# Performance work log

Hardware: AMD Instinct MI355X
Metric: run time of the kernel (lower is better)

The kernel has to match this reference:

```python
import jax, jax.numpy as jnp
import numpy as np

EMBED_DIM = 1024
NUM_HEADS = 16
HEAD_DIM = EMBED_DIM // NUM_HEADS
BATCH = 2
SEQ = 2048


def setup_inputs() -> dict:
    key = jax.random.key(0)
    ks = jax.random.split(key, 7)
    bound = 1.0 / np.sqrt(EMBED_DIM)  # nn.Linear default init range
    x = jax.random.normal(ks[0], (BATCH, SEQ, EMBED_DIM), dtype=jnp.float32)
    attn_mask = jnp.ones((BATCH, SEQ), dtype=jnp.int32)
    Wq = jax.random.uniform(ks[1], (EMBED_DIM, EMBED_DIM), jnp.float32, -bound, bound)
    bq = jax.random.uniform(ks[2], (EMBED_DIM,), jnp.float32, -bound, bound)
    Wk = jax.random.uniform(ks[3], (EMBED_DIM, EMBED_DIM), jnp.float32, -bound, bound)
    bk = jax.random.uniform(ks[4], (EMBED_DIM,), jnp.float32, -bound, bound)
    Wv = jax.random.uniform(ks[5], (EMBED_DIM, EMBED_DIM), jnp.float32, -bound, bound)
    bv = jax.random.uniform(ks[6], (EMBED_DIM,), jnp.float32, -bound, bound)
    return {"x": x, "attn_mask": attn_mask, "inv_scale": 8,
            "Wq": Wq, "bq": bq, "Wk": Wk, "bk": bk, "Wv": Wv, "bv": bv}


def reference(x, attn_mask, inv_scale, Wq, bq, Wk, bk, Wv, bv):
    bs, seq_len, _ = x.shape
    # Linear layers (torch: y = x @ W.T + b; here W stored as [in,out])
    def split_heads(y):
        return y.reshape(bs, seq_len, NUM_HEADS, HEAD_DIM).transpose(0, 2, 1, 3)  # [b,h,s,d]
    q = split_heads(x @ Wq + bq)
    k = split_heads(x @ Wk + bk)
    v = split_heads(x @ Wv + bv)
    scores = jnp.einsum('bhqd,bhkd->bhqk', q, k) / jnp.asarray(inv_scale, x.dtype)
    mask = (attn_mask == 0)[:, None, None, :]  # True where masked
    scores = jnp.where(mask, -jnp.inf, scores)
    attn = jax.nn.softmax(scores, axis=-1)
    out = jnp.einsum('bhqk,bhkd->bhqd', attn, v)  # [b,h,s,d]
    return out
```

## Files before the change

kernel.cpp:

```cpp
#include <hip/hip_runtime.h>
#include <stdint.h>

typedef __bf16 bf16x8 __attribute__((ext_vector_type(8)));
typedef float f32x4 __attribute__((ext_vector_type(4)));
typedef uint32_t u32x2 __attribute__((ext_vector_type(2)));
typedef uint32_t u32x4 __attribute__((ext_vector_type(4)));

#define MFMA16(a, b, c) __builtin_amdgcn_mfma_f32_16x16x32_bf16((a), (b), (c), 0, 0, 0)

#if __has_builtin(__builtin_amdgcn_exp2f)
#define EXP2F(x) __builtin_amdgcn_exp2f(x)
#else
#define EXP2F(x) exp2f(x)
#endif

__device__ __forceinline__ void gload16(const void* gsrc, void* ldst) {
  __builtin_amdgcn_global_load_lds((__attribute__((address_space(1))) void*)gsrc,
                                   (__attribute__((address_space(3))) void*)ldst, 16, 0, 0);
}

__device__ __forceinline__ uint32_t pkbf(float a, float b) {
  uint16_t ua = __builtin_bit_cast(uint16_t, (__bf16)a);
  uint16_t ub = __builtin_bit_cast(uint16_t, (__bf16)b);
  return (uint32_t)ua | ((uint32_t)ub << 16);
}

__global__ __launch_bounds__(256) void prep_kernel(
    const float* __restrict__ x, const float* __restrict__ Wq,
    const float* __restrict__ Wk, const float* __restrict__ Wv,
    ushort* __restrict__ xb, ushort* __restrict__ wt) {
  int tid = blockIdx.x * 256 + threadIdx.x;
  if (tid < 524288) {
    const f32x4* xp = (const f32x4*)x;
    f32x4 a = xp[tid * 2], b = xp[tid * 2 + 1];
    u32x4 o;
    o[0] = pkbf(a[0], a[1]);
    o[1] = pkbf(a[2], a[3]);
    o[2] = pkbf(b[0], b[1]);
    o[3] = pkbf(b[2], b[3]);
    *(u32x4*)(xb + (size_t)tid * 8) = o;
  } else {
    int r = tid - 524288;
    int mtx = r >> 17;
    int q = r & 131071;
    int n = q & 1023, kc = q >> 10;
    const float* W = (mtx == 0) ? Wq : (mtx == 1) ? Wk : Wv;
    const float* src = W + (size_t)kc * 8 * 1024 + n;
    float v0 = src[0], v1 = src[1024], v2 = src[2048], v3 = src[3072];
    float v4 = src[4096], v5 = src[5120], v6 = src[6144], v7 = src[7168];
    u32x4 o;
    o[0] = pkbf(v0, v1);
    o[1] = pkbf(v2, v3);
    o[2] = pkbf(v4, v5);
    o[3] = pkbf(v6, v7);
    *(u32x4*)(wt + (size_t)mtx * 1048576 + (size_t)n * 1024 + kc * 8) = o;
  }
}

__global__ __launch_bounds__(256, 2) void gemm_qkv(
    const ushort* __restrict__ xb, const ushort* __restrict__ wt,
    const float* __restrict__ bq, const float* __restrict__ bk,
    const float* __restrict__ bv, const int* __restrict__ invp,
    ushort* __restrict__ Qb, ushort* __restrict__ Kb, ushort* __restrict__ Vt) {
  __shared__ ushort ash[2][128 * 64];
  __shared__ ushort bsh[2][128 * 64];
  const int tid = threadIdx.x;
  const int w = tid >> 6, l = tid & 63;
  const int lq = l & 15, g = l >> 4;

  const int f = blockIdx.x;
  const int nf = (f & 7) * 96 + (f >> 3);
  const int bx = nf / 24, byy = nf % 24;
  const int z = byy >> 3;
  const int m0 = bx * 128, n0 = (byy & 7) * 128;

  const ushort* A = xb;
  const ushort* B = wt + (size_t)z * 1048576;
  const float* bias = (z == 0) ? bq : (z == 1) ? bk : bv;
  const float qs = 1.44269504088896341f / (float)(invp[0]);

  const int lr = l >> 3;
  const int scol = ((l & 7) * 8) ^ (lr * 8);
  const int wr = w >> 1, wc = w & 1;
  const int swz = (lq & 7) << 4;

  f32x4 acc[4][4] = {};

  auto stage = [&](int nb, int t) {
    int k0 = t * 64;
#pragma unroll
    for (int i = 0; i < 4; ++i) {
      int row = w * 32 + i * 8;
      gload16(A + (size_t)(m0 + row + lr) * 1024 + k0 + scol, &ash[nb][row * 64]);
    }
#pragma unroll
    for (int i = 0; i < 4; ++i) {
      int row = w * 32 + i * 8;
      gload16(B + (size_t)(n0 + row + lr) * 1024 + k0 + scol, &bsh[nb][row * 64]);
    }
  };

  stage(0, 0);
  __syncthreads();
  int buf = 0;
  for (int t = 0; t < 16; ++t) {
    if (t < 15) stage(buf ^ 1, t + 1);
    bf16x8 af[4][2], bfr[4][2];
#pragma unroll
    for (int mi = 0; mi < 4; ++mi)
#pragma unroll
      for (int kk = 0; kk < 2; ++kk) {
        int row = wr * 64 + mi * 16 + lq;
        af[mi][kk] = *(const bf16x8*)((const char*)&ash[buf][0] + row * 128 +
                                      ((kk * 64 + g * 16) ^ swz));
      }
#pragma unroll
    for (int ni = 0; ni < 4; ++ni)
#pragma unroll
      for (int kk = 0; kk < 2; ++kk) {
        int row = wc * 64 + ni * 16 + lq;
        bfr[ni][kk] = *(const bf16x8*)((const char*)&bsh[buf][0] + row * 128 +
                                       ((kk * 64 + g * 16) ^ swz));
      }
#pragma unroll
    for (int mi = 0; mi < 4; ++mi)
#pragma unroll
      for (int ni = 0; ni < 4; ++ni) {
        acc[mi][ni] = MFMA16(af[mi][0], bfr[ni][0], acc[mi][ni]);
        acc[mi][ni] = MFMA16(af[mi][1], bfr[ni][1], acc[mi][ni]);
      }
    __syncthreads();
    buf ^= 1;
  }

#pragma unroll
  for (int ni = 0; ni < 4; ++ni) {
    int nn = n0 + wc * 64 + ni * 16 + lq;
    int h = nn >> 6, d = nn & 63;
    float bb = bias[nn];
#pragma unroll
    for (int mi = 0; mi < 4; ++mi) {
      int mbase = m0 + wr * 64 + mi * 16 + g * 4;
      if (z < 2) {
        ushort* dst = (z == 0) ? Qb : Kb;
#pragma unroll
        for (int j = 0; j < 4; ++j) {
          int mm = mbase + j;
          int b = mm >> 11, s = mm & 2047;
          float v = acc[mi][ni][j] + bb;
          if (z == 0) v *= qs;
          dst[((size_t)(b * 16 + h) * 2048 + s) * 64 + d] =
              __builtin_bit_cast(uint16_t, (__bf16)v);
        }
      } else {
        int b = mbase >> 11, s0 = mbase & 2047;
        u32x2 pk;
        pk[0] = pkbf(acc[mi][ni][0] + bb, acc[mi][ni][1] + bb);
        pk[1] = pkbf(acc[mi][ni][2] + bb, acc[mi][ni][3] + bb);
        *(u32x2*)(Vt + ((size_t)(b * 16 + h) * 64 + d) * 2048 + s0) = pk;
      }
    }
  }
}

__global__ __launch_bounds__(256, 4) void attn_kernel(
    const ushort* __restrict__ Qb, const ushort* __restrict__ Kb,
    const ushort* __restrict__ Vt, const int* __restrict__ mask,
    float* __restrict__ out) {
  __shared__ ushort ksh[2][64 * 64];
  __shared__ ushort vsh[2][64 * 64];
  __shared__ ushort psh[4][16 * 64];
  const int tid = threadIdx.x;
  const int w = tid >> 6, l = tid & 63;
  const int lq = l & 15, g = l >> 4;

  const int f = blockIdx.x;
  const int nf = ((f & 7) << 7) + (f >> 3);
  const int qt = nf & 31, bh = nf >> 5;
  const int b = bh >> 4;

  const ushort* Qp = Qb + ((size_t)bh * 2048 + qt * 64 + w * 16) * 64;
  const ushort* Kp = Kb + (size_t)bh * 2048 * 64;
  const ushort* Vp = Vt + (size_t)bh * 64 * 2048;
  const int* mp = mask + b * 2048;

  const int lr = l >> 3;
  const int scol = ((l & 7) * 8) ^ (lr * 8);
  const int swz = (lq & 7) << 4;

  bf16x8 qf_[2];
#pragma unroll
  for (int kk = 0; kk < 2; ++kk)
    qf_[kk] = *(const bf16x8*)(Qp + lq * 64 + kk * 32 + g * 8);

  f32x4 acco[4] = {};
  float m_ = -__builtin_inff();
  float l_ = 0.f;

  auto stage = [&](int nb, int t) {
#pragma unroll
    for (int i = 0; i < 2; ++i) {
      int row = w * 16 + i * 8;
      gload16(Kp + (size_t)(t * 64 + row + lr) * 64 + scol, &ksh[nb][row * 64]);
      gload16(Vp + (size_t)(row + lr) * 2048 + t * 64 + scol, &vsh[nb][row * 64]);
    }
  };
  stage(0, 0);
  __syncthreads();
  int buf = 0;
  for (int t = 0; t < 32; ++t) {
    if (t < 31) stage(buf ^ 1, t + 1);
    bf16x8 kf_[4][2];
#pragma unroll
    for (int kf = 0; kf < 4; ++kf)
#pragma unroll
      for (int kk = 0; kk < 2; ++kk) {
        int row = kf * 16 + lq;
        kf_[kf][kk] = *(const bf16x8*)((const char*)&ksh[buf][0] + row * 128 +
                                       ((kk * 64 + g * 16) ^ swz));
      }
    f32x4 sc[4];
    __builtin_amdgcn_s_setprio(1);
#pragma unroll
    for (int kf = 0; kf < 4; ++kf) {
      f32x4 zz = {0.f, 0.f, 0.f, 0.f};
      zz = MFMA16(kf_[kf][0], qf_[0], zz);
      sc[kf] = MFMA16(kf_[kf][1], qf_[1], zz);
    }
    __builtin_amdgcn_s_setprio(0);
    int4 mv[4];
#pragma unroll
    for (int kf = 0; kf < 4; ++kf)
      mv[kf] = *(const int4*)(mp + t * 64 + kf * 16 + g * 4);
    float mx = -__builtin_inff();
#pragma unroll
    for (int kf = 0; kf < 4; ++kf)
#pragma unroll
      for (int j = 0; j < 4; ++j) mx = fmaxf(mx, sc[kf][j]);
    mx = fmaxf(mx, __shfl_xor(mx, 16, 64));
    mx = fmaxf(mx, __shfl_xor(mx, 32, 64));
    if (!__all(mx - m_ <= 8.f)) {
      float mnew = fmaxf(m_, mx);
      float alpha = EXP2F(m_ - mnew);
      m_ = mnew;
      l_ *= alpha;
#pragma unroll
      for (int nd = 0; nd < 4; ++nd) acco[nd] *= alpha;
    }
    float ps = 0.f;
    char* pbase = (char*)&psh[w][0] + lq * 128;
#pragma unroll
    for (int kf = 0; kf < 4; ++kf) {
      float pv[4];
#pragma unroll
      for (int j = 0; j < 4; ++j) {
        float e = EXP2F(sc[kf][j] - m_);
        int mm = (j == 0) ? mv[kf].x : (j == 1) ? mv[kf].y : (j == 2) ? mv[kf].z : mv[kf].w;
        e = mm ? e : 0.f;
        pv[j] = e;
        ps += e;
      }
      u32x2 pk2;
      pk2[0] = pkbf(pv[0], pv[1]);
      pk2[1] = pkbf(pv[2], pv[3]);
      *(u32x2*)(pbase + ((kf * 32 + g * 8) ^ swz)) = pk2;
    }
    ps += __shfl_xor(ps, 16, 64);
    ps += __shfl_xor(ps, 32, 64);
    l_ += ps;
    bf16x8 pf[2], vf[4][2];
#pragma unroll
    for (int kc = 0; kc < 2; ++kc)
      pf[kc] = *(const bf16x8*)((const char*)&psh[w][0] + lq * 128 +
                                ((kc * 64 + g * 16) ^ swz));
#pragma unroll
    for (int nd = 0; nd < 4; ++nd)
#pragma unroll
      for (int kc = 0; kc < 2; ++kc) {
        int row = nd * 16 + lq;
        vf[nd][kc] = *(const bf16x8*)((const char*)&vsh[buf][0] + row * 128 +
                                      ((kc * 64 + g * 16) ^ swz));
      }
    __builtin_amdgcn_s_setprio(1);
#pragma unroll
    for (int nd = 0; nd < 4; ++nd) {
      acco[nd] = MFMA16(vf[nd][0], pf[0], acco[nd]);
      acco[nd] = MFMA16(vf[nd][1], pf[1], acco[nd]);
    }
    __builtin_amdgcn_s_setprio(0);
    __syncthreads();
    buf ^= 1;
  }
  float r = 1.0f / l_;
  int qrow = qt * 64 + w * 16 + lq;
#pragma unroll
  for (int nd = 0; nd < 4; ++nd) {
    f32x4 v = acco[nd] * r;
    int d0 = nd * 16 + g * 4;
    *(f32x4*)(out + ((size_t)bh * 2048 + qrow) * 64 + d0) = v;
  }
}

extern "C" void kernel_launch(void* const* d_in, const int* in_sizes, int n_in,
                              void* d_out, int out_size, void* d_ws,
                              size_t ws_size, hipStream_t stream) {
  (void)in_sizes; (void)n_in; (void)out_size; (void)ws_size;
  const float* x = (const float*)d_in[0];
  const int* mask = (const int*)d_in[1];
  const int* invp = (const int*)d_in[2];
  const float* Wq = (const float*)d_in[3];
  const float* bq = (const float*)d_in[4];
  const float* Wk = (const float*)d_in[5];
  const float* bk = (const float*)d_in[6];
  const float* Wv = (const float*)d_in[7];
  const float* bv = (const float*)d_in[8];

  ushort* xb = (ushort*)d_ws;
  ushort* wt = xb + 4194304;
  ushort* Qb = wt + 3145728;
  ushort* Kb = Qb + 4194304;
  ushort* Vt = Kb + 4194304;
  float* out = (float*)d_out;

  prep_kernel<<<3584, 256, 0, stream>>>(x, Wq, Wk, Wv, xb, wt);
  gemm_qkv<<<768, 256, 0, stream>>>(xb, wt, bq, bk, bv, invp, Qb, Kb, Vt);
  attn_kernel<<<1024, 256, 0, stream>>>(Qb, Kb, Vt, mask, out);
}
```

Measured before the change: 199.3 us.

## Fold mask into additive bias, keep P in registers, single-buffer QKV GEMM

The prep kernel now turns the int mask into an additive float bias (0 or -1e30), which becomes the initial accumulator of the QK^T MFMA, so the per-element mask select goes away. The attention kernel drops its LDS round trip for P and instead reorders the probabilities in registers with v_permlane32/16_swap, and it computes the row sum with an extra MFMA against a ones vector. The GEMM moves from double to single buffering with an extra barrier, raising occupancy from 2 to 3 blocks, and attention launch bounds go from 4 to 5. The risks are less load/compute overlap in the GEMM and the correctness of the lane permutation, which relies on gfx950 permlane instructions.

New measurement: 219.7 us. 1.1x slower.

```diff
diff --git a/kernel.cpp b/kernel.cpp
--- a/kernel.cpp
+++ b/kernel.cpp
@@ -28,7 +28,8 @@
 __global__ __launch_bounds__(256) void prep_kernel(
     const float* __restrict__ x, const float* __restrict__ Wq,
     const float* __restrict__ Wk, const float* __restrict__ Wv,
-    ushort* __restrict__ xb, ushort* __restrict__ wt) {
+    const int* __restrict__ mask, ushort* __restrict__ xb,
+    ushort* __restrict__ wt, float* __restrict__ biasf) {
   int tid = blockIdx.x * 256 + threadIdx.x;
   if (tid < 524288) {
     const f32x4* xp = (const f32x4*)x;
@@ -39,7 +40,7 @@
     o[2] = pkbf(b[0], b[1]);
     o[3] = pkbf(b[2], b[3]);
     *(u32x4*)(xb + (size_t)tid * 8) = o;
-  } else {
+  } else if (tid < 917504) {
     int r = tid - 524288;
     int mtx = r >> 17;
     int q = r & 131071;
@@ -54,16 +55,25 @@
     o[2] = pkbf(v4, v5);
     o[3] = pkbf(v6, v7);
     *(u32x4*)(wt + (size_t)mtx * 1048576 + (size_t)n * 1024 + kc * 8) = o;
-  }
-}
-
-__global__ __launch_bounds__(256, 2) void gemm_qkv(
+  } else {
+    int r = tid - 917504;
+    int4 mv = *(const int4*)(mask + r * 4);
+    f32x4 o;
+    o[0] = mv.x ? 0.f : -1e30f;
+    o[1] = mv.y ? 0.f : -1e30f;
+    o[2] = mv.z ? 0.f : -1e30f;
+    o[3] = mv.w ? 0.f : -1e30f;
+    *(f32x4*)(biasf + r * 4) = o;
+  }
+}
+
+__global__ __launch_bounds__(256, 3) void gemm_qkv(
     const ushort* __restrict__ xb, const ushort* __restrict__ wt,
     const float* __restrict__ bq, const float* __restrict__ bk,
     const float* __restrict__ bv, const int* __restrict__ invp,
     ushort* __restrict__ Qb, ushort* __restrict__ Kb, ushort* __restrict__ Vt) {
-  __shared__ ushort ash[2][128 * 64];
-  __shared__ ushort bsh[2][128 * 64];
+  __shared__ ushort ash[128 * 64];
+  __shared__ ushort bsh[128 * 64];
   const int tid = threadIdx.x;
   const int w = tid >> 6, l = tid & 63;
   const int lq = l & 15, g = l >> 4;
@@ -86,32 +96,30 @@
 
   f32x4 acc[4][4] = {};
 
-  auto stage = [&](int nb, int t) {
+  auto stage = [&](int t) {
     int k0 = t * 64;
 #pragma unroll
     for (int i = 0; i < 4; ++i) {
       int row = w * 32 + i * 8;
-      gload16(A + (size_t)(m0 + row + lr) * 1024 + k0 + scol, &ash[nb][row * 64]);
+      gload16(A + (size_t)(m0 + row + lr) * 1024 + k0 + scol, &ash[row * 64]);
     }
 #pragma unroll
     for (int i = 0; i < 4; ++i) {
       int row = w * 32 + i * 8;
-      gload16(B + (size_t)(n0 + row + lr) * 1024 + k0 + scol, &bsh[nb][row * 64]);
+      gload16(B + (size_t)(n0 + row + lr) * 1024 + k0 + scol, &bsh[row * 64]);
     }
   };
 
-  stage(0, 0);
+  stage(0);
   __syncthreads();
-  int buf = 0;
   for (int t = 0; t < 16; ++t) {
-    if (t < 15) stage(buf ^ 1, t + 1);
     bf16x8 af[4][2], bfr[4][2];
 #pragma unroll
     for (int mi = 0; mi < 4; ++mi)
 #pragma unroll
       for (int kk = 0; kk < 2; ++kk) {
         int row = wr * 64 + mi * 16 + lq;
-        af[mi][kk] = *(const bf16x8*)((const char*)&ash[buf][0] + row * 128 +
+        af[mi][kk] = *(const bf16x8*)((const char*)&ash[0] + row * 128 +
                                       ((kk * 64 + g * 16) ^ swz));
       }
 #pragma unroll
@@ -119,9 +127,12 @@
 #pragma unroll
       for (int kk = 0; kk < 2; ++kk) {
         int row = wc * 64 + ni * 16 + lq;
-        bfr[ni][kk] = *(const bf16x8*)((const char*)&bsh[buf][0] + row * 128 +
+        bfr[ni][kk] = *(const bf16x8*)((const char*)&bsh[0] + row * 128 +
                                        ((kk * 64 + g * 16) ^ swz));
       }
+    __syncthreads();
+    if (t < 15) stage(t + 1);
+    __builtin_amdgcn_s_setprio(1);
 #pragma unroll
     for (int mi = 0; mi < 4; ++mi)
 #pragma unroll
@@ -129,8 +140,8 @@
         acc[mi][ni] = MFMA16(af[mi][0], bfr[ni][0], acc[mi][ni]);
         acc[mi][ni] = MFMA16(af[mi][1], bfr[ni][1], acc[mi][ni]);
       }
+    __builtin_amdgcn_s_setprio(0);
     __syncthreads();
-    buf ^= 1;
   }
 
 #pragma unroll
@@ -163,16 +174,16 @@
   }
 }
 
-__global__ __launch_bounds__(256, 4) void attn_kernel(
+__global__ __launch_bounds__(256, 5) void attn_kernel(
     const ushort* __restrict__ Qb, const ushort* __restrict__ Kb,
-    const ushort* __restrict__ Vt, const int* __restrict__ mask,
+    const ushort* __restrict__ Vt, const float* __restrict__ biasf,
     float* __restrict__ out) {
   __shared__ ushort ksh[2][64 * 64];
   __shared__ ushort vsh[2][64 * 64];
-  __shared__ ushort psh[4][16 * 64];
   const int tid = threadIdx.x;
   const int w = tid >> 6, l = tid & 63;
   const int lq = l & 15, g = l >> 4;
+  const bool hi16 = (l & 16) != 0;
 
   const int f = blockIdx.x;
   const int nf = ((f & 7) << 7) + (f >> 3);
@@ -182,7 +193,7 @@
   const ushort* Qp = Qb + ((size_t)bh * 2048 + qt * 64 + w * 16) * 64;
   const ushort* Kp = Kb + (size_t)bh * 2048 * 64;
   const ushort* Vp = Vt + (size_t)bh * 64 * 2048;
-  const int* mp = mask + b * 2048;
+  const float* bp = biasf + b * 2048;
 
   const int lr = l >> 3;
   const int scol = ((l & 7) * 8) ^ (lr * 8);
@@ -193,9 +204,16 @@
   for (int kk = 0; kk < 2; ++kk)
     qf_[kk] = *(const bf16x8*)(Qp + lq * 64 + kk * 32 + g * 8);
 
+  bf16x8 ones_;
+  {
+    __bf16 o = (lq == 0) ? (__bf16)1.0f : (__bf16)0.0f;
+#pragma unroll
+    for (int i = 0; i < 8; ++i) ones_[i] = o;
+  }
+
   f32x4 acco[4] = {};
+  f32x4 accl = {0.f, 0.f, 0.f, 0.f};
   float m_ = -__builtin_inff();
-  float l_ = 0.f;
 
   auto stage = [&](int nb, int t) {
 #pragma unroll
@@ -210,6 +228,10 @@
   int buf = 0;
   for (int t = 0; t < 32; ++t) {
     if (t < 31) stage(buf ^ 1, t + 1);
+    f32x4 bias4[4];
+#pragma unroll
+    for (int kf = 0; kf < 4; ++kf)
+      bias4[kf] = *(const f32x4*)(bp + t * 64 + kf * 16 + g * 4);
     bf16x8 kf_[4][2];
 #pragma unroll
     for (int kf = 0; kf < 4; ++kf)
@@ -223,75 +245,76 @@
     __builtin_amdgcn_s_setprio(1);
 #pragma unroll
     for (int kf = 0; kf < 4; ++kf) {
-      f32x4 zz = {0.f, 0.f, 0.f, 0.f};
-      zz = MFMA16(kf_[kf][0], qf_[0], zz);
+      f32x4 zz = MFMA16(kf_[kf][0], qf_[0], bias4[kf]);
       sc[kf] = MFMA16(kf_[kf][1], qf_[1], zz);
     }
     __builtin_amdgcn_s_setprio(0);
-    int4 mv[4];
-#pragma unroll
-    for (int kf = 0; kf < 4; ++kf)
-      mv[kf] = *(const int4*)(mp + t * 64 + kf * 16 + g * 4);
-    float mx = -__builtin_inff();
-#pragma unroll
-    for (int kf = 0; kf < 4; ++kf)
-#pragma unroll
-      for (int j = 0; j < 4; ++j) mx = fmaxf(mx, sc[kf][j]);
+    bf16x8 vf[4][2];
+#pragma unroll
+    for (int nd = 0; nd < 4; ++nd)
+#pragma unroll
+      for (int kc = 0; kc < 2; ++kc) {
+        int row = nd * 16 + lq;
+        vf[nd][kc] = *(const bf16x8*)((const char*)&vsh[buf][0] + row * 128 +
+                                      ((kc * 64 + g * 16) ^ swz));
+      }
+    float t0 = fmaxf(fmaxf(sc[0][0], sc[0][1]), sc[0][2]);
+    float t1 = fmaxf(fmaxf(sc[0][3], sc[1][0]), sc[1][1]);
+    float t2 = fmaxf(fmaxf(sc[1][2], sc[1][3]), sc[2][0]);
+    float t3 = fmaxf(fmaxf(sc[2][1], sc[2][2]), sc[2][3]);
+    float t4 = fmaxf(fmaxf(sc[3][0], sc[3][1]), sc[3][2]);
+    float mx = fmaxf(fmaxf(fmaxf(t0, t1), t2), fmaxf(fmaxf(t3, t4), sc[3][3]));
     mx = fmaxf(mx, __shfl_xor(mx, 16, 64));
     mx = fmaxf(mx, __shfl_xor(mx, 32, 64));
     if (!__all(mx - m_ <= 8.f)) {
       float mnew = fmaxf(m_, mx);
       float alpha = EXP2F(m_ - mnew);
       m_ = mnew;
-      l_ *= alpha;
+      accl *= alpha;
 #pragma unroll
       for (int nd = 0; nd < 4; ++nd) acco[nd] *= alpha;
     }
-    float ps = 0.f;
-    char* pbase = (char*)&psh[w][0] + lq * 128;
+    uint32_t Wp[4][2];
 #pragma unroll
     for (int kf = 0; kf < 4; ++kf) {
-      float pv[4];
-#pragma unroll
-      for (int j = 0; j < 4; ++j) {
-        float e = EXP2F(sc[kf][j] - m_);
-        int mm = (j == 0) ? mv[kf].x : (j == 1) ? mv[kf].y : (j == 2) ? mv[kf].z : mv[kf].w;
-        e = mm ? e : 0.f;
-        pv[j] = e;
-        ps += e;
-      }
-      u32x2 pk2;
-      pk2[0] = pkbf(pv[0], pv[1]);
-      pk2[1] = pkbf(pv[2], pv[3]);
-      *(u32x2*)(pbase + ((kf * 32 + g * 8) ^ swz)) = pk2;
-    }
-    ps += __shfl_xor(ps, 16, 64);
-    ps += __shfl_xor(ps, 32, 64);
-    l_ += ps;
-    bf16x8 pf[2], vf[4][2];
+      float e0 = EXP2F(sc[kf][0] - m_);
+      float e1 = EXP2F(sc[kf][1] - m_);
+      float e2 = EXP2F(sc[kf][2] - m_);
+      float e3 = EXP2F(sc[kf][3] - m_);
+      Wp[kf][0] = pkbf(e0, e1);
+      Wp[kf][1] = pkbf(e2, e3);
+    }
+    u32x4 R[2];
 #pragma unroll
     for (int kc = 0; kc < 2; ++kc)
-      pf[kc] = *(const bf16x8*)((const char*)&psh[w][0] + lq * 128 +
-                                ((kc * 64 + g * 16) ^ swz));
-#pragma unroll
-    for (int nd = 0; nd < 4; ++nd)
-#pragma unroll
-      for (int kc = 0; kc < 2; ++kc) {
-        int row = nd * 16 + lq;
-        vf[nd][kc] = *(const bf16x8*)((const char*)&vsh[buf][0] + row * 128 +
-                                      ((kc * 64 + g * 16) ^ swz));
-      }
+#pragma unroll
+      for (int wd = 0; wd < 2; ++wd) {
+        uint32_t X = Wp[2 * kc][wd], Y = Wp[2 * kc + 1][wd];
+        asm volatile("v_permlane32_swap_b32 %0, %1" : "+v"(X), "+v"(Y));
+        uint32_t Xd = X, Xs = X;
+        asm volatile("v_permlane16_swap_b32 %0, %1" : "+v"(Xd), "+v"(Xs));
+        uint32_t Yd = Y, Ys = Y;
+        asm volatile("v_permlane16_swap_b32 %0, %1" : "+v"(Yd), "+v"(Ys));
+        R[kc][wd] = hi16 ? Yd : X;
+        R[kc][2 + wd] = hi16 ? Y : Xs;
+      }
+    bf16x8 pf[2];
+    pf[0] = __builtin_bit_cast(bf16x8, R[0]);
+    pf[1] = __builtin_bit_cast(bf16x8, R[1]);
     __builtin_amdgcn_s_setprio(1);
 #pragma unroll
     for (int nd = 0; nd < 4; ++nd) {
       acco[nd] = MFMA16(vf[nd][0], pf[0], acco[nd]);
       acco[nd] = MFMA16(vf[nd][1], pf[1], acco[nd]);
     }
+    accl = MFMA16(ones_, pf[0], accl);
+    accl = MFMA16(ones_, pf[1], accl);
     __builtin_amdgcn_s_setprio(0);
     __syncthreads();
     buf ^= 1;
   }
-  float r = 1.0f / l_;
+  float ls = __shfl(accl[0], lq, 64);
+  float r = 1.0f / ls;
   int qrow = qt * 64 + w * 16 + lq;
 #pragma unroll
   for (int nd = 0; nd < 4; ++nd) {
@@ -320,9 +343,10 @@
   ushort* Qb = wt + 3145728;
   ushort* Kb = Qb + 4194304;
   ushort* Vt = Kb + 4194304;
+  float* biasf = (float*)(Vt + 4194304);
   float* out = (float*)d_out;
 
-  prep_kernel<<<3584, 256, 0, stream>>>(x, Wq, Wk, Wv, xb, wt);
+  prep_kernel<<<3588, 256, 0, stream>>>(x, Wq, Wk, Wv, mask, xb, wt, biasf);
   gemm_qkv<<<768, 256, 0, stream>>>(xb, wt, bq, bk, bv, invp, Qb, Kb, Vt);
-  attn_kernel<<<1024, 256, 0, stream>>>(Qb, Kb, Vt, mask, out);
-}
+  attn_kernel<<<1024, 256, 0, stream>>>(Qb, Kb, Vt, biasf, out);
+}
```
